# Kernel optimization log

Hardware: AMD Instinct MI355X
Metric: run time of the kernel (lower is better)

Reference implementation:

```python
import jax, jax.numpy as jnp
import numpy as np

P = 128; D = 128; A = 128
NS = D * A            # sinogram nodes
NP = P * P            # pixel nodes
N = NS + NP           # total graph nodes
EPS = 1e-5
_PNAMES = ["af_w1","af_b1","af_p1","af_bn_g","af_bn_b","af_w2","af_b2","af_p2","af_w3","af_b3","af_p3","af_w4","af_b4","af_p4","af_w5","af_b5","af_p5","gcn_w","gcn_b","sr_w1","sr_b1","sr_p1","sr_w2","sr_b2","sr_p2","sr_w3","sr_b3","sr_p3"]


def _conv(x, w, b, pad):
    y = jax.lax.conv_general_dilated(x, w, (1, 1), [(pad, pad), (pad, pad)],
                                     dimension_numbers=("NCHW", "OIHW", "NCHW"))
    return y + b[None, :, None, None]


def _prelu(x, a):
    return jnp.where(x >= 0, x, a * x)


def _bn(x, g, b):
    # BatchNorm2d in training mode: biased batch stats over (N,H,W)
    m = x.mean(axis=(0, 2, 3), keepdims=True)
    v = x.var(axis=(0, 2, 3), keepdims=True)
    return (x - m) * jax.lax.rsqrt(v + EPS) * g[None, :, None, None] + b[None, :, None, None]


def _forward(sino, edge_index, edge_weight, p):
    # AndrewCNN sinogram filter: 1 -> 64 -> 64 -> 64 -> 64 -> 8, 7x7 convs
    h = _prelu(_conv(sino, p["af_w1"], p["af_b1"], 3), p["af_p1"])
    h = _bn(h, p["af_bn_g"], p["af_bn_b"])
    h = _prelu(_conv(h, p["af_w2"], p["af_b2"], 3), p["af_p2"])
    h = _prelu(_conv(h, p["af_w3"], p["af_b3"], 3), p["af_p3"])
    h = _prelu(_conv(h, p["af_w4"], p["af_b4"], 3), p["af_p4"])
    h = _prelu(_conv(h, p["af_w5"], p["af_b5"], 3), p["af_p5"])   # [B,8,D,A]
    B, F = h.shape[0], h.shape[1]
    # build_nodes_features (source_to_target): sino nodes first, zero pixel nodes
    flat_sino = h.transpose(0, 2, 3, 1).reshape(B, NS, F)
    x = jnp.concatenate([flat_sino, jnp.zeros((B, NP, F), h.dtype)], axis=1)  # [B,N,8]
    # GCNConv(8,10): lin -> gcn_norm with self loops -> scatter-add at targets -> +bias
    xl = x @ p["gcn_w"]                                            # [B,N,10]
    row, col = edge_index[0], edge_index[1]
    loop = jnp.arange(N)
    row2 = jnp.concatenate([row, loop])
    col2 = jnp.concatenate([col, loop])
    w2 = jnp.concatenate([edge_weight, jnp.ones((N,), edge_weight.dtype)])
    deg = jnp.zeros((N,), xl.dtype).at[col2].add(w2)
    dis = jnp.where(deg > 0, jax.lax.rsqrt(jnp.maximum(deg, EPS * 0 + 1e-30)), 0.0)
    norm = dis[row2] * w2 * dis[col2]                              # [E+N]
    msgs = xl[:, row2, :] * norm[None, :, None]                    # [B,E+N,10]
    agg = jnp.zeros_like(xl).at[:, col2, :].add(msgs) + p["gcn_b"]
    # keep pixel nodes, reshape to image grid
    img = agg[:, NS:, :].transpose(0, 2, 1).reshape(B, -1, P, P)   # [B,10,P,P]
    # SRNET: 10 -> 64 (9x9) -> 32 (1x1) -> 1 (5x5)
    o = _prelu(_conv(img, p["sr_w1"], p["sr_b1"], 4), p["sr_p1"])
    o = _prelu(_conv(o,   p["sr_w2"], p["sr_b2"], 0), p["sr_p2"])
    o = _prelu(_conv(o,   p["sr_w3"], p["sr_b3"], 2), p["sr_p3"])
    return o


def setup_inputs() -> dict:
    f = jnp.float32
    ks = jax.random.split(jax.random.key(0), 16)
    B, E = 4, 2097152
    def rn(k, shape, s):
        return jax.random.normal(k, shape, f) * s
    inp = {
        "sino": jax.random.normal(ks[0], (B, 1, D, A), f),
        "edge_index": jax.random.randint(ks[1], (2, E), 0, N),
        "edge_weight": jax.random.uniform(ks[2], (E,), f),
    }
    kw = jax.random.split(ks[3], 9)
    inp["af_w1"] = rn(kw[0], (64, 1, 7, 7), 0.2)
    inp["af_w2"] = rn(kw[1], (64, 64, 7, 7), 0.03)
    inp["af_w3"] = rn(kw[2], (64, 64, 7, 7), 0.03)
    inp["af_w4"] = rn(kw[3], (64, 64, 7, 7), 0.03)
    inp["af_w5"] = rn(kw[4], (8, 64, 7, 7), 0.03)
    inp["gcn_w"] = rn(kw[5], (8, 10), 0.3)
    inp["sr_w1"] = rn(kw[6], (64, 10, 9, 9), 0.05)
    inp["sr_w2"] = rn(kw[7], (32, 64, 1, 1), 0.18)
    inp["sr_w3"] = rn(kw[8], (1, 32, 5, 5), 0.05)
    for nm, c in [("af_b1", 64), ("af_b2", 64), ("af_b3", 64), ("af_b4", 64), ("af_b5", 8), ("sr_b1", 64), ("sr_b2", 32), ("sr_b3", 1)]:
        inp[nm] = jnp.zeros((c,), f)
    inp["gcn_b"] = jnp.zeros((10,), f)
    inp["af_bn_g"] = jnp.ones((64,), f)
    inp["af_bn_b"] = jnp.zeros((64,), f)
    for nm in ["af_p1", "af_p2", "af_p3", "af_p4", "af_p5", "sr_p1", "sr_p2", "sr_p3"]:
        inp[nm] = jnp.array(0.25, f)
    return inp


def reference(sino, edge_index, edge_weight, af_w1, af_b1, af_p1, af_bn_g, af_bn_b, af_w2, af_b2, af_p2, af_w3, af_b3, af_p3, af_w4, af_b4, af_p4, af_w5, af_b5, af_p5, gcn_w, gcn_b, sr_w1, sr_b1, sr_p1, sr_w2, sr_b2, sr_p2, sr_w3, sr_b3, sr_p3):
    p = dict(zip(_PNAMES, (af_w1, af_b1, af_p1, af_bn_g, af_bn_b, af_w2, af_b2, af_p2, af_w3, af_b3, af_p3, af_w4, af_b4, af_p4, af_w5, af_b5, af_p5, gcn_w, gcn_b, sr_w1, sr_b1, sr_p1, sr_w2, sr_b2, sr_p2, sr_w3, sr_b3, sr_p3)))
    return _forward(sino, edge_index, edge_weight, p)
```

## Files before the change

### kernel.cpp

```cpp
#include <hip/hip_runtime.h>

static constexpr int NS = 16384;

typedef __attribute__((ext_vector_type(8))) short bf16x8;
typedef __attribute__((ext_vector_type(4))) float f32x4;

__device__ inline unsigned short bf16_rne(float x) {
  unsigned u = __float_as_uint(x);
  unsigned r = u + 0x7FFF + ((u >> 16) & 1);
  return (unsigned short)(r >> 16);
}

__global__ void k_wtrans(const float* __restrict__ w, float* __restrict__ wT,
                         int CO, int CI_IN, int CI_OUT, int KS) {
  int i = blockIdx.x * 256 + threadIdx.x;
  int tot = KS * KS * CI_OUT * CO;
  if (i >= tot) return;
  int co = i % CO;
  int r = i / CO;
  int ci = r % CI_OUT;
  int t = r / CI_OUT;
  int ky = t / KS, kx = t % KS;
  float v = 0.f;
  if (ci < CI_IN) v = w[((co * CI_IN + ci) * KS + ky) * KS + kx];
  wT[i] = v;
}

__global__ void k_wpack(const float* __restrict__ w, unsigned short* __restrict__ wpk) {
  int i = blockIdx.x * 256 + threadIdx.x;
  if (i >= 49 * 64 * 64) return;
  int co = i & 63, r = i >> 6;
  int ci = r & 63, tap = r >> 6;
  float v = w[(co * 64 + ci) * 49 + tap];
  unsigned short hi = bf16_rne(v);
  float hif = __uint_as_float((unsigned)hi << 16);
  unsigned short lo = bf16_rne(v - hif);
  int ks = ci >> 5, k32 = ci & 31;
  int lane = ((k32 >> 3) << 4) | (co & 15);
  int j = ci & 7, nt = co >> 4;
  size_t base = ((size_t)(((tap * 2 + ks) * 4 + nt) * 2) * 64 + lane) * 8 + j;
  wpk[base] = hi;
  wpk[base + 512] = lo;
}

__global__ void k_wpacks(const float* __restrict__ sw1,
                         unsigned short* __restrict__ wpk) {
  int i = blockIdx.x * 256 + threadIdx.x;
  if (i >= 360 * 512) return;
  int j = i & 7, l = (i >> 3) & 63, f = i >> 9;
  int sp = f & 1, nt = (f >> 1) & 3;
  int r3 = f >> 3, p = r3 % 5, ky = r3 / 5;
  int co = nt * 16 + (l & 15);
  int k = ((l >> 4) << 3) + j;
  int kx = 2 * p + (k >> 4);
  int ci = k & 15;
  float v = (ci < 10 && kx < 9) ? sw1[((co * 10 + ci) * 9 + ky) * 9 + kx] : 0.f;
  unsigned short hi = bf16_rne(v);
  unsigned short outv;
  if (sp == 0) {
    outv = hi;
  } else {
    float hif = __uint_as_float((unsigned)hi << 16);
    outv = bf16_rne(v - hif);
  }
  wpk[i] = outv;
}

__global__ __launch_bounds__(128) void k_conv1(
    const float* __restrict__ sino, const float* __restrict__ wT1,
    const float* __restrict__ b1, const float* __restrict__ p1,
    float* __restrict__ out) {
  int b = blockIdx.x >> 7, y = blockIdx.x & 127, x = threadIdx.x;
  float acc[64];
#pragma unroll
  for (int i = 0; i < 64; ++i) acc[i] = 0.f;
#pragma unroll
  for (int ky = 0; ky < 7; ++ky) {
    int yy = y + ky - 3;
#pragma unroll
    for (int kx = 0; kx < 7; ++kx) {
      int xx = x + kx - 3;
      float v = (yy >= 0 && yy < 128 && xx >= 0 && xx < 128)
                    ? sino[(b * 128 + yy) * 128 + xx]
                    : 0.f;
      const float* wr = wT1 + (ky * 7 + kx) * 64;
#pragma unroll
      for (int co = 0; co < 64; ++co) acc[co] += v * wr[co];
    }
  }
  float a = p1[0];
  float* op = out + ((size_t)(b * 134 + y + 3) * 134 + x + 3) * 64;
#pragma unroll
  for (int co = 0; co < 64; ++co) {
    float v = acc[co] + b1[co];
    op[co] = v >= 0.f ? v : a * v;
  }
}

__global__ __launch_bounds__(256) void k_bnstats(const float* __restrict__ x1p,
                                                 double* __restrict__ bnsum) {
  int c = threadIdx.x & 63, sl = threadIdx.x >> 6;
  double s = 0.0, q = 0.0;
  int base = blockIdx.x * 512 + sl * 128;
  for (int i = 0; i < 128; ++i) {
    int p = base + i;
    int b = p >> 14, y = (p >> 7) & 127, x = p & 127;
    double v = (double)x1p[((size_t)(b * 134 + y + 3) * 134 + x + 3) * 64 + c];
    s += v;
    q += v * v;
  }
  __shared__ double red[2][4][64];
  red[0][sl][c] = s;
  red[1][sl][c] = q;
  __syncthreads();
  if (sl == 0) {
    s = red[0][0][c] + red[0][1][c] + red[0][2][c] + red[0][3][c];
    q = red[1][0][c] + red[1][1][c] + red[1][2][c] + red[1][3][c];
    atomicAdd(&bnsum[c], s);
    atomicAdd(&bnsum[64 + c], q);
  }
}

__global__ void k_bnfinal(const double* __restrict__ bnsum, float* __restrict__ bnsc,
                          const float* __restrict__ g, const float* __restrict__ bb) {
  int c = threadIdx.x;
  if (c >= 64) return;
  double m = bnsum[c] * (1.0 / 65536.0);
  double v = bnsum[64 + c] * (1.0 / 65536.0) - m * m;
  double sc = (double)g[c] * rsqrt(v + 1e-5);
  bnsc[c] = (float)sc;
  bnsc[64 + c] = (float)((double)bb[c] - m * sc);
}

__global__ __launch_bounds__(256) void k_bnapply(float* __restrict__ x1p,
                                                 const float* __restrict__ bnsc) {
  int i = blockIdx.x * 256 + threadIdx.x;
  if (i >= 4 * 128 * 128 * 16) return;
  int g = i & 15, p = i >> 4;
  int b = p >> 14, y = (p >> 7) & 127, x = p & 127;
  float* ptr = x1p + ((size_t)(b * 134 + y + 3) * 134 + x + 3) * 64 + g * 4;
  float4 v = *(float4*)ptr;
  int c = g * 4;
  v.x = v.x * bnsc[c + 0] + bnsc[64 + c + 0];
  v.y = v.y * bnsc[c + 1] + bnsc[64 + c + 1];
  v.z = v.z * bnsc[c + 2] + bnsc[64 + c + 2];
  v.w = v.w * bnsc[c + 3] + bnsc[64 + c + 3];
  *(float4*)ptr = v;
}

__global__ __launch_bounds__(256) void k_convm(
    const float* __restrict__ in, const unsigned short* __restrict__ wpk,
    const float* __restrict__ bias, const float* __restrict__ alpha,
    float* __restrict__ out) {
  int b = blockIdx.x >> 7, y = blockIdx.x & 127;
  int tid = threadIdx.x, l = tid & 63;
  int wv = tid >> 6;
  int pxb = (wv & 1) * 64;
  int coh = wv >> 1;
  int lg = l >> 4, lm = l & 15;

  __shared__ unsigned short hbuf[2][134 * 40];
  __shared__ unsigned short lbuf[2][134 * 40];

  f32x4 acc[4][2];
#pragma unroll
  for (int mt = 0; mt < 4; ++mt)
#pragma unroll
    for (int ntl = 0; ntl < 2; ++ntl) acc[mt][ntl] = (f32x4){0.f, 0.f, 0.f, 0.f};

  for (int ch = 0; ch < 64; ch += 32) {
    auto stage = [&](int ky, int s) {
      const float* gin = in + ((size_t)(b * 134 + y + ky) * 134) * 64 + ch;
      for (int i = tid; i < 134 * 8; i += 256) {
        int px = i >> 3, q = i & 7;
        float4 v = *(const float4*)(gin + px * 64 + q * 4);
        unsigned short h0 = bf16_rne(v.x), h1 = bf16_rne(v.y);
        unsigned short h2 = bf16_rne(v.z), h3 = bf16_rne(v.w);
        unsigned short l0 = bf16_rne(v.x - __uint_as_float((unsigned)h0 << 16));
        unsigned short l1 = bf16_rne(v.y - __uint_as_float((unsigned)h1 << 16));
        unsigned short l2 = bf16_rne(v.z - __uint_as_float((unsigned)h2 << 16));
        unsigned short l3 = bf16_rne(v.w - __uint_as_float((unsigned)h3 << 16));
        *(ushort4*)&hbuf[s][px * 40 + q * 4] = make_ushort4(h0, h1, h2, h3);
        *(ushort4*)&lbuf[s][px * 40 + q * 4] = make_ushort4(l0, l1, l2, l3);
      }
    };
    stage(0, 0);
    __syncthreads();
    for (int ky = 0; ky < 7; ++ky) {
      if (ky < 6) stage(ky + 1, (ky + 1) & 1);
      int s = ky & 1;
#pragma unroll
      for (int kx = 0; kx < 7; ++kx) {
        int tap = ky * 7 + kx;
        const unsigned short* wt =
            wpk + (size_t)(tap * 2 + (ch >> 5)) * 8 * 512 + (size_t)l * 8;
        bf16x8 Bh[2], Bl[2];
#pragma unroll
        for (int ntl = 0; ntl < 2; ++ntl) {
          int nt = coh * 2 + ntl;
          Bh[ntl] = *(const bf16x8*)(wt + (nt * 2 + 0) * 512);
          Bl[ntl] = *(const bf16x8*)(wt + (nt * 2 + 1) * 512);
        }
#pragma unroll
        for (int mt = 0; mt < 4; ++mt) {
          int px = pxb + mt * 16 + lm + kx;
          bf16x8 Ah = *(const bf16x8*)&hbuf[s][px * 40 + lg * 8];
          bf16x8 Al = *(const bf16x8*)&lbuf[s][px * 40 + lg * 8];
#pragma unroll
          for (int ntl = 0; ntl < 2; ++ntl) {
            acc[mt][ntl] = __builtin_amdgcn_mfma_f32_16x16x32_bf16(Ah, Bh[ntl],
                                                                   acc[mt][ntl], 0, 0, 0);
            acc[mt][ntl] = __builtin_amdgcn_mfma_f32_16x16x32_bf16(Ah, Bl[ntl],
                                                                   acc[mt][ntl], 0, 0, 0);
            acc[mt][ntl] = __builtin_amdgcn_mfma_f32_16x16x32_bf16(Al, Bh[ntl],
                                                                   acc[mt][ntl], 0, 0, 0);
          }
        }
      }
      __syncthreads();
    }
  }
  float a = alpha[0];
#pragma unroll
  for (int mt = 0; mt < 4; ++mt)
#pragma unroll
    for (int ntl = 0; ntl < 2; ++ntl)
#pragma unroll
      for (int r = 0; r < 4; ++r) {
        int px = pxb + mt * 16 + lg * 4 + r;
        int co = coh * 32 + ntl * 16 + lm;
        float v = acc[mt][ntl][r] + bias[co];
        out[((size_t)(b * 134 + y + 3) * 134 + px + 3) * 64 + co] =
            v >= 0.f ? v : a * v;
      }
}

__global__ __launch_bounds__(256) void k_convs(
    const float* __restrict__ imgp, const unsigned short* __restrict__ wpk,
    const float* __restrict__ bias, const float* __restrict__ alpha,
    float* __restrict__ out) {
  int b = blockIdx.x >> 7, y = blockIdx.x & 127;
  int tid = threadIdx.x, l = tid & 63;
  int wv = tid >> 6, wbase = wv * 32;
  int lg = l >> 4, lm = l & 15;

  __shared__ unsigned short hbuf[2][137 * 20];
  __shared__ unsigned short lbuf[2][137 * 20];

  f32x4 acc[2][4];
#pragma unroll
  for (int mt = 0; mt < 2; ++mt)
#pragma unroll
    for (int nt = 0; nt < 4; ++nt) acc[mt][nt] = (f32x4){0.f, 0.f, 0.f, 0.f};

  auto stage = [&](int ky, int s) {
    const float* gin = imgp + ((size_t)(b * 136 + y + ky) * 136) * 16;
    for (int i = tid; i < 137 * 4; i += 256) {
      int px = i >> 2, q = i & 3;
      float4 v = (px < 136) ? *(const float4*)(gin + px * 16 + q * 4)
                            : make_float4(0.f, 0.f, 0.f, 0.f);
      unsigned short h0 = bf16_rne(v.x), h1 = bf16_rne(v.y);
      unsigned short h2 = bf16_rne(v.z), h3 = bf16_rne(v.w);
      unsigned short l0 = bf16_rne(v.x - __uint_as_float((unsigned)h0 << 16));
      unsigned short l1 = bf16_rne(v.y - __uint_as_float((unsigned)h1 << 16));
      unsigned short l2 = bf16_rne(v.z - __uint_as_float((unsigned)h2 << 16));
      unsigned short l3 = bf16_rne(v.w - __uint_as_float((unsigned)h3 << 16));
      *(ushort4*)&hbuf[s][px * 20 + q * 4] = make_ushort4(h0, h1, h2, h3);
      *(ushort4*)&lbuf[s][px * 20 + q * 4] = make_ushort4(l0, l1, l2, l3);
    }
  };
  stage(0, 0);
  __syncthreads();
  for (int ky = 0; ky < 9; ++ky) {
    if (ky < 8) stage(ky + 1, (ky + 1) & 1);
    int s = ky & 1;
#pragma unroll
    for (int p = 0; p < 5; ++p) {
      const unsigned short* wt =
          wpk + ((size_t)(ky * 5 + p) * 8) * 512 + (size_t)l * 8;
      bf16x8 Bh[4], Bl[4];
#pragma unroll
      for (int nt = 0; nt < 4; ++nt) {
        Bh[nt] = *(const bf16x8*)(wt + (nt * 2 + 0) * 512);
        Bl[nt] = *(const bf16x8*)(wt + (nt * 2 + 1) * 512);
      }
#pragma unroll
      for (int mt = 0; mt < 2; ++mt) {
        int px = wbase + mt * 16 + lm + 2 * p + (lg >> 1);
        bf16x8 Ah = *(const bf16x8*)&hbuf[s][px * 20 + (lg & 1) * 8];
        bf16x8 Al = *(const bf16x8*)&lbuf[s][px * 20 + (lg & 1) * 8];
#pragma unroll
        for (int nt = 0; nt < 4; ++nt) {
          acc[mt][nt] =
              __builtin_amdgcn_mfma_f32_16x16x32_bf16(Ah, Bh[nt], acc[mt][nt], 0, 0, 0);
          acc[mt][nt] =
              __builtin_amdgcn_mfma_f32_16x16x32_bf16(Ah, Bl[nt], acc[mt][nt], 0, 0, 0);
          acc[mt][nt] =
              __builtin_amdgcn_mfma_f32_16x16x32_bf16(Al, Bh[nt], acc[mt][nt], 0, 0, 0);
        }
      }
    }
    __syncthreads();
  }
  float a = alpha[0];
#pragma unroll
  for (int mt = 0; mt < 2; ++mt)
#pragma unroll
    for (int nt = 0; nt < 4; ++nt)
#pragma unroll
      for (int r = 0; r < 4; ++r) {
        int px = wbase + mt * 16 + lg * 4 + r;
        int co = nt * 16 + lm;
        float v = acc[mt][nt][r] + bias[co];
        out[((size_t)(b * 128 + y) * 128 + px) * 64 + co] = v >= 0.f ? v : a * v;
      }
}

template <int CIN, int COUT, int KS, int IN_H, int IN_W, int OUT_H, int OUT_W,
          int OUT_OFF, int STR, int CH, int NSPLIT>
__global__ __launch_bounds__(64 * NSPLIT) void k_conv3(
    const float* __restrict__ in, const float* __restrict__ wT,
    const float* __restrict__ bias, const float* __restrict__ alpha,
    float* __restrict__ out) {
  constexpr int C = COUT / NSPLIT;
  int b = blockIdx.x >> 6, y0 = (blockIdx.x & 63) * 2;
  int l = threadIdx.x & 63;
  int cob = __builtin_amdgcn_readfirstlane((int)(threadIdx.x >> 6) * C);
  __shared__ float sbuf[2][IN_W * STR];
  float acc[4][C];
#pragma unroll
  for (int r = 0; r < 4; ++r)
#pragma unroll
    for (int i = 0; i < C; ++i) acc[r][i] = 0.f;

  for (int ch = 0; ch < CIN; ch += CH) {
    auto stage = [&](int k) {
      const float* gin = in + ((size_t)(b * IN_H + y0 + k) * IN_W) * CIN + ch;
      float* dst = sbuf[k & 1];
      constexpr int N4 = IN_W * CH / 4;
      for (int i = threadIdx.x; i < N4; i += 64 * NSPLIT) {
        int xx = i / (CH / 4), c4 = (i - xx * (CH / 4)) * 4;
        float4 v = *(const float4*)(gin + (size_t)xx * CIN + c4);
        *(float4*)(dst + xx * STR + c4) = v;
      }
    };
    stage(0);
    stage(1);
    __syncthreads();
    for (int ky = 0; ky < KS; ++ky) {
      const float* sA = sbuf[ky & 1];
      const float* sB = sbuf[(ky + 1) & 1];
      for (int kx = 0; kx < KS; ++kx) {
        const float* wt = wT + ((size_t)(ky * KS + kx) * CIN + ch) * COUT + cob;
        const float* a0p = sA + (l + kx) * STR;
        const float* a1p = sA + (l + 64 + kx) * STR;
        const float* b0p = sB + (l + kx) * STR;
        const float* b1p = sB + (l + 64 + kx) * STR;
#pragma unroll
        for (int ci = 0; ci < CH; ci += 4) {
          float4 a0 = *(const float4*)(a0p + ci);
          float4 a1 = *(const float4*)(a1p + ci);
          float4 b0 = *(const float4*)(b0p + ci);
          float4 b1 = *(const float4*)(b1p + ci);
#pragma unroll
          for (int c = 0; c < 4; ++c) {
            const float* wr = wt + (size_t)(ci + c) * COUT;
            float va0 = ((const float*)&a0)[c], va1 = ((const float*)&a1)[c];
            float vb0 = ((const float*)&b0)[c], vb1 = ((const float*)&b1)[c];
#pragma unroll
            for (int co = 0; co < C; ++co) {
              float w = wr[co];
              acc[0][co] += va0 * w;
              acc[1][co] += va1 * w;
              acc[2][co] += vb0 * w;
              acc[3][co] += vb1 * w;
            }
          }
        }
      }
      __syncthreads();
      if (ky < KS - 1) {
        stage(ky + 2);
        __syncthreads();
      }
    }
  }
  float a = alpha[0];
#pragma unroll
  for (int r = 0; r < 2; ++r) {
    float* rowp =
        out + (((size_t)(b * OUT_H + y0 + r + OUT_OFF)) * OUT_W + OUT_OFF) * COUT + cob;
#pragma unroll
    for (int p = 0; p < 2; ++p) {
      float* op = rowp + (size_t)(l + p * 64) * COUT;
#pragma unroll
      for (int co = 0; co < C; ++co) {
        float v = acc[r * 2 + p][co] + bias[cob + co];
        op[co] = v >= 0.f ? v : a * v;
      }
    }
  }
}

template <int CIN, int COUT, int KS, int IN_H, int IN_W, int OUT_H, int OUT_W,
          int OUT_OFF, int STR, int NSPLIT>
__global__ __launch_bounds__(64 * NSPLIT) void k_conv2(
    const float* __restrict__ in, const float* __restrict__ wT,
    const float* __restrict__ bias, const float* __restrict__ alpha,
    float* __restrict__ out) {
  constexpr int C = COUT / NSPLIT;
  int b = blockIdx.x >> 7, y = blockIdx.x & 127;
  int l = threadIdx.x & 63;
  int cob = __builtin_amdgcn_readfirstlane((int)(threadIdx.x >> 6) * C);
  __shared__ float srow[IN_W * STR];
  float acc0[C], acc1[C];
#pragma unroll
  for (int i = 0; i < C; ++i) acc0[i] = acc1[i] = 0.f;

  for (int ky = 0; ky < KS; ++ky) {
    __syncthreads();
    const float* gin = in + (size_t)(b * IN_H + y + ky) * IN_W * CIN;
    constexpr int N4 = IN_W * CIN / 4;
    for (int i = threadIdx.x; i < N4; i += 64 * NSPLIT) {
      float4 v = *(const float4*)(gin + (size_t)i * 4);
      int xx = (i * 4) / CIN, cc = (i * 4) % CIN;
      *(float4*)(srow + xx * STR + cc) = v;
    }
    __syncthreads();
    for (int kx = 0; kx < KS; ++kx) {
      const float* wt = wT + ((size_t)(ky * KS + kx) * CIN) * COUT + cob;
      const float* s0 = srow + (l + kx) * STR;
      const float* s1 = srow + (l + 64 + kx) * STR;
      for (int ci = 0; ci < CIN; ci += 4) {
        float4 a0 = *(const float4*)(s0 + ci);
        float4 a1 = *(const float4*)(s1 + ci);
#pragma unroll
        for (int c = 0; c < 4; ++c) {
          float v0 = ((const float*)&a0)[c];
          float v1 = ((const float*)&a1)[c];
          const float* wr = wt + (size_t)(ci + c) * COUT;
#pragma unroll
          for (int co = 0; co < C; ++co) {
            float w = wr[co];
            acc0[co] += v0 * w;
            acc1[co] += v1 * w;
          }
        }
      }
    }
  }
  float a = alpha[0];
  float* rowp = out + ((size_t)(b * OUT_H + y + OUT_OFF) * OUT_W + OUT_OFF) * COUT + cob;
  float* op0 = rowp + (size_t)l * COUT;
  float* op1 = rowp + (size_t)(l + 64) * COUT;
#pragma unroll
  for (int co = 0; co < C; ++co) {
    float bi = bias[cob + co];
    float v0 = acc0[co] + bi;
    float v1 = acc1[co] + bi;
    op0[co] = v0 >= 0.f ? v0 : a * v0;
    op1[co] = v1 >= 0.f ? v1 : a * v1;
  }
}

__global__ __launch_bounds__(512, 4) void k_conv5gcn(
    const float* __restrict__ in, const float* __restrict__ wT5,
    const float* __restrict__ b5, const float* __restrict__ p5,
    const float* __restrict__ gw, float* __restrict__ xl) {
  int b = blockIdx.x >> 7, y = blockIdx.x & 127;
  int x = threadIdx.x & 127;
  int cig = __builtin_amdgcn_readfirstlane((int)(threadIdx.x >> 7));
  __shared__ float srow[134 * 68];
  __shared__ float red[4][128][8];
  float acc[8];
#pragma unroll
  for (int i = 0; i < 8; ++i) acc[i] = 0.f;

  for (int ky = 0; ky < 7; ++ky) {
    __syncthreads();
    const float* gin = in + (size_t)(b * 134 + y + ky) * 134 * 64;
    for (int i = threadIdx.x; i < 134 * 64; i += 512) {
      int xx = i >> 6, cc = i & 63;
      srow[xx * 68 + cc] = gin[i];
    }
    __syncthreads();
    for (int kx = 0; kx < 7; ++kx) {
      const float* wt = wT5 + (size_t)(ky * 7 + kx) * 64 * 8 + cig * 16 * 8;
      const float* sr = srow + (x + kx) * 68 + cig * 16;
#pragma unroll
      for (int ci = 0; ci < 16; ci += 4) {
        float4 iv = *(const float4*)(sr + ci);
#pragma unroll
        for (int c = 0; c < 4; ++c) {
          float vv = ((const float*)&iv)[c];
          const float* wr = wt + (ci + c) * 8;
#pragma unroll
          for (int co = 0; co < 8; ++co) acc[co] += vv * wr[co];
        }
      }
    }
  }
#pragma unroll
  for (int co = 0; co < 8; ++co) red[cig][x][co] = acc[co];
  __syncthreads();
  if (cig == 0) {
    float a = p5[0];
    float feat[8];
#pragma unroll
    for (int co = 0; co < 8; ++co) {
      float v = red[0][x][co] + red[1][x][co] + red[2][x][co] + red[3][x][co] + b5[co];
      feat[co] = v >= 0.f ? v : a * v;
    }
    float o[10];
#pragma unroll
    for (int f = 0; f < 10; ++f) o[f] = 0.f;
#pragma unroll
    for (int c = 0; c < 8; ++c) {
#pragma unroll
      for (int f = 0; f < 10; ++f) o[f] += feat[c] * gw[c * 10 + f];
    }
    float* op = xl + ((size_t)b * 16384 + y * 128 + x) * 10;
#pragma unroll
    for (int f = 0; f < 10; ++f) op[f] = o[f];
  }
}

template <int HALF>
__global__ __launch_bounds__(1024) void k_degp(
    const int* __restrict__ ei, const float* __restrict__ ew,
    float* __restrict__ pdeg, int* __restrict__ cnt, int* __restrict__ rank, int E) {
  __shared__ float degl[16384];
  for (int i = threadIdx.x; i < 16384; i += 1024) degl[i] = 0.f;
  __syncthreads();
  int chunk = (E + gridDim.x - 1) / gridDim.x;
  int base = blockIdx.x * chunk;
  int end = min(E, base + chunk);
  for (int e = base + (int)threadIdx.x; e < end; e += 1024) {
    int col = ei[E + e];
    float w = ew[e];
    if ((col >> 14) == HALF) atomicAdd(&degl[col & 16383], w);
    if (HALF == 1) {
      int row = ei[e];
      if (row < NS && col >= NS) rank[e] = atomicAdd(&cnt[col - NS], 1);
    }
  }
  __syncthreads();
  float* pd = pdeg + (size_t)blockIdx.x * 16384;
  for (int i = threadIdx.x; i < 16384; i += 1024) pd[i] = degl[i];
}

__global__ void k_dis2(const float* __restrict__ pdegA, const float* __restrict__ pdegB,
                       float* __restrict__ dis, int nb) {
  int n = blockIdx.x * 256 + threadIdx.x;
  if (n >= 2 * NS) return;
  const float* p = (n < NS ? pdegA : pdegB) + (n & 16383);
  float s = 1.0f;
  for (int b = 0; b < nb; ++b) s += p[(size_t)b * 16384];
  dis[n] = rsqrtf(s);
}

__global__ __launch_bounds__(1024) void k_scan(const int* __restrict__ cnt,
                                               int* __restrict__ ptr) {
  __shared__ int ps[1024];
  int tid = threadIdx.x;
  int base = tid * 16;
  int v[16];
  int s = 0;
#pragma unroll
  for (int k = 0; k < 16; ++k) {
    v[k] = s;
    s += cnt[base + k];
  }
  ps[tid] = s;
  __syncthreads();
  for (int off = 1; off < 1024; off <<= 1) {
    int t = (tid >= off) ? ps[tid - off] : 0;
    __syncthreads();
    ps[tid] += t;
    __syncthreads();
  }
  int chunkoff = (tid == 0) ? 0 : ps[tid - 1];
#pragma unroll
  for (int k = 0; k < 16; ++k) ptr[base + k] = chunkoff + v[k];
  if (tid == 1023) ptr[16384] = ps[1023];
}

__global__ void k_bucket2(const int* __restrict__ ei, const float* __restrict__ ew,
                          const float* __restrict__ dis, const int* __restrict__ ptr,
                          const int* __restrict__ rank, int* __restrict__ erow,
                          float* __restrict__ enrm, int E) {
  int e = blockIdx.x * 256 + threadIdx.x;
  if (e >= E) return;
  int row = ei[e], col = ei[E + e];
  if (row >= NS || col < NS) return;
  int cp = col - NS;
  int pos = ptr[cp] + rank[e];
  erow[pos] = row;
  enrm[pos] = dis[row] * ew[e] * dis[col];
}

__global__ __launch_bounds__(256) void k_gather(
    const int* __restrict__ ptr, const int* __restrict__ erow,
    const float* __restrict__ enrm, const float* __restrict__ xl,
    const float* __restrict__ gb, float* __restrict__ imgp) {
  int cp = blockIdx.x * 4 + (threadIdx.x >> 6);
  int l = threadIdx.x & 63;
  int b = l >> 4, f = l & 15;
  bool act = f < 10;
  float acc = 0.f;
  int s = ptr[cp], e1 = ptr[cp + 1];
  for (int e = s; e < e1; ++e) {
    int row = erow[e];
    float nrm = enrm[e];
    if (act) acc += xl[((size_t)b * 16384 + row) * 10 + f] * nrm;
  }
  if (act) {
    int y = cp >> 7, x = cp & 127;
    imgp[((size_t)(b * 136 + y + 4) * 136 + x + 4) * 16 + f] = acc + gb[f];
  }
}

extern "C" void kernel_launch(void* const* d_in, const int* in_sizes, int n_in,
                              void* d_out, int out_size, void* d_ws, size_t ws_size,
                              hipStream_t stream) {
  const float* sino = (const float*)d_in[0];
  const int* ei = (const int*)d_in[1];
  const float* ew = (const float*)d_in[2];
  const float* w1 = (const float*)d_in[3];
  const float* w2 = (const float*)d_in[4];
  const float* w3 = (const float*)d_in[5];
  const float* w4 = (const float*)d_in[6];
  const float* w5 = (const float*)d_in[7];
  const float* gw = (const float*)d_in[8];
  const float* sw1 = (const float*)d_in[9];
  const float* sw2 = (const float*)d_in[10];
  const float* sw3 = (const float*)d_in[11];
  const float* b1 = (const float*)d_in[12];
  const float* b2 = (const float*)d_in[13];
  const float* b3 = (const float*)d_in[14];
  const float* b4 = (const float*)d_in[15];
  const float* b5 = (const float*)d_in[16];
  const float* sb1 = (const float*)d_in[17];
  const float* sb2 = (const float*)d_in[18];
  const float* sb3 = (const float*)d_in[19];
  const float* gb = (const float*)d_in[20];
  const float* bng = (const float*)d_in[21];
  const float* bnb = (const float*)d_in[22];
  const float* p1 = (const float*)d_in[23];
  const float* p2 = (const float*)d_in[24];
  const float* p3 = (const float*)d_in[25];
  const float* p4 = (const float*)d_in[26];
  const float* p5 = (const float*)d_in[27];
  const float* sp1 = (const float*)d_in[28];
  const float* sp2 = (const float*)d_in[29];
  const float* sp3 = (const float*)d_in[30];
  const int E = in_sizes[2];

  char* ws = (char*)d_ws;
  size_t off = 0;
  auto alloc = [&](size_t bytes) {
    char* p = ws + off;
    off += (bytes + 255) & ~(size_t)255;
    return p;
  };
  float* x1p = (float*)alloc((size_t)4 * 134 * 134 * 64 * 4);
  float* x2p = (float*)alloc((size_t)4 * 134 * 134 * 64 * 4);
  unsigned short* wpk2 = (unsigned short*)alloc(401408 * 2);
  unsigned short* wpk3 = (unsigned short*)alloc(401408 * 2);
  unsigned short* wpk4 = (unsigned short*)alloc(401408 * 2);
  unsigned short* wpks1 = (unsigned short*)alloc(184320 * 2);
  float* wt1 = (float*)alloc(3136 * 4);
  float* wt5 = (float*)alloc(25088 * 4);
  float* wts2 = (float*)alloc(2048 * 4);
  float* wts3 = (float*)alloc(800 * 4);
  double* bnsum = (double*)alloc(128 * 8);
  float* bnsc = (float*)alloc(128 * 4);
  float* xl = (float*)alloc((size_t)4 * 16384 * 10 * 4);
  float* pdegA = (float*)alloc((size_t)128 * 16384 * 4);
  float* pdegB = (float*)alloc((size_t)128 * 16384 * 4);
  float* dis = (float*)alloc(32768 * 4);
  int* cnt = (int*)alloc(16384 * 4);
  int* ptr = (int*)alloc(16385 * 4);
  int* rank = (int*)alloc((size_t)E * 4);
  int* erow = (int*)alloc((size_t)E * 4);
  float* enrm = (float*)alloc((size_t)E * 4);
  float* imgp = (float*)alloc((size_t)4 * 136 * 136 * 16 * 4);
  float* s1 = (float*)alloc((size_t)4 * 128 * 128 * 64 * 4);
  float* s2p = (float*)alloc((size_t)4 * 132 * 132 * 32 * 4);

  hipMemsetAsync(x1p, 0, (size_t)4 * 134 * 134 * 64 * 4, stream);
  hipMemsetAsync(x2p, 0, (size_t)4 * 134 * 134 * 64 * 4, stream);
  hipMemsetAsync(bnsum, 0, 128 * 8, stream);
  hipMemsetAsync(cnt, 0, 16384 * 4, stream);
  hipMemsetAsync(imgp, 0, (size_t)4 * 136 * 136 * 16 * 4, stream);
  hipMemsetAsync(s2p, 0, (size_t)4 * 132 * 132 * 32 * 4, stream);

  k_wpack<<<784, 256, 0, stream>>>(w2, wpk2);
  k_wpack<<<784, 256, 0, stream>>>(w3, wpk3);
  k_wpack<<<784, 256, 0, stream>>>(w4, wpk4);
  k_wpacks<<<720, 256, 0, stream>>>(sw1, wpks1);
  k_wtrans<<<13, 256, 0, stream>>>(w1, wt1, 64, 1, 1, 7);
  k_wtrans<<<98, 256, 0, stream>>>(w5, wt5, 8, 64, 64, 7);
  k_wtrans<<<8, 256, 0, stream>>>(sw2, wts2, 32, 64, 64, 1);
  k_wtrans<<<4, 256, 0, stream>>>(sw3, wts3, 1, 32, 32, 5);

  k_conv1<<<512, 128, 0, stream>>>(sino, wt1, b1, p1, x1p);
  k_bnstats<<<128, 256, 0, stream>>>(x1p, bnsum);
  k_bnfinal<<<1, 64, 0, stream>>>(bnsum, bnsc, bng, bnb);
  k_bnapply<<<4096, 256, 0, stream>>>(x1p, bnsc);

  k_convm<<<512, 256, 0, stream>>>(x1p, wpk2, b2, p2, x2p);
  k_convm<<<512, 256, 0, stream>>>(x2p, wpk3, b3, p3, x1p);
  k_convm<<<512, 256, 0, stream>>>(x1p, wpk4, b4, p4, x2p);
  k_conv5gcn<<<512, 512, 0, stream>>>(x2p, wt5, b5, p5, gw, xl);

  k_degp<0><<<128, 1024, 0, stream>>>(ei, ew, pdegA, cnt, rank, E);
  k_degp<1><<<128, 1024, 0, stream>>>(ei, ew, pdegB, cnt, rank, E);
  k_dis2<<<128, 256, 0, stream>>>(pdegA, pdegB, dis, 128);
  k_scan<<<1, 1024, 0, stream>>>(cnt, ptr);
  k_bucket2<<<(E + 255) / 256, 256, 0, stream>>>(ei, ew, dis, ptr, rank, erow, enrm, E);
  k_gather<<<4096, 256, 0, stream>>>(ptr, erow, enrm, xl, gb, imgp);

  k_convs<<<512, 256, 0, stream>>>(imgp, wpks1, sb1, sp1, s1);
  k_conv3<64, 32, 1, 128, 128, 132, 132, 2, 36, 32, 8>
      <<<256, 512, 0, stream>>>(s1, wts2, sb2, sp2, s2p);
  k_conv2<32, 1, 5, 132, 132, 128, 128, 0, 36, 1>
      <<<512, 64, 0, stream>>>(s2p, wts3, sb3, sp3, (float*)d_out);
}
```

Measured before the change: 670.1 us.

## Move conv5 (64->8, 7x7) onto bf16x3 MFMA with split-precision weight packing

Replaces the scalar FP32 conv5+GCN-linear kernel with an MFMA kernel. Inputs are split into bf16 hi/lo parts in double-buffered shared memory, and three 16x16x32 bf16 MFMAs per tap emulate fp32 accuracy. Output channels are padded from 8 to 16, so half of the MFMA columns are wasted. Adds a new weight-packing kernel, and the per-row staging conversion adds ALU work.

```diff
diff --git a/kernel.cpp b/kernel.cpp
--- a/kernel.cpp
+++ b/kernel.cpp
@@ -41,6 +41,28 @@
   size_t base = ((size_t)(((tap * 2 + ks) * 4 + nt) * 2) * 64 + lane) * 8 + j;
   wpk[base] = hi;
   wpk[base + 512] = lo;
+}
+
+__global__ void k_wpack5(const float* __restrict__ w5,
+                         unsigned short* __restrict__ wpk) {
+  int i = blockIdx.x * 256 + threadIdx.x;
+  if (i >= 196 * 512) return;
+  int j = i & 7, l = (i >> 3) & 63, f = i >> 9;
+  int sp = f & 1, r = f >> 1;
+  int ks = r & 1, tap = r >> 1;
+  int co = l & 15;
+  int k32 = ((l >> 4) << 3) + j;
+  int ci = ks * 32 + k32;
+  float v = (co < 8) ? w5[(co * 64 + ci) * 49 + tap] : 0.f;
+  unsigned short hi = bf16_rne(v);
+  unsigned short outv;
+  if (sp == 0) {
+    outv = hi;
+  } else {
+    float hif = __uint_as_float((unsigned)hi << 16);
+    outv = bf16_rne(v - hif);
+  }
+  wpk[i] = outv;
 }
 
 __global__ void k_wpacks(const float* __restrict__ sw1,
@@ -235,6 +257,94 @@
       }
 }
 
+__global__ __launch_bounds__(256) void k_convm5(
+    const float* __restrict__ in, const unsigned short* __restrict__ wpk,
+    const float* __restrict__ b5, const float* __restrict__ p5,
+    const float* __restrict__ gw, float* __restrict__ xl) {
+  int b = blockIdx.x >> 7, y = blockIdx.x & 127;
+  int tid = threadIdx.x, l = tid & 63;
+  int wv = tid >> 6;
+  int pxb = wv * 32;
+  int lg = l >> 4, lm = l & 15;
+
+  __shared__ unsigned short hbuf[2][134 * 40];
+  __shared__ unsigned short lbuf[2][134 * 40];
+  __shared__ float feat[128][9];
+
+  f32x4 acc[2];
+  acc[0] = (f32x4){0.f, 0.f, 0.f, 0.f};
+  acc[1] = (f32x4){0.f, 0.f, 0.f, 0.f};
+
+  for (int ch = 0; ch < 64; ch += 32) {
+    auto stage = [&](int ky, int s) {
+      const float* gin = in + ((size_t)(b * 134 + y + ky) * 134) * 64 + ch;
+      for (int i = tid; i < 134 * 8; i += 256) {
+        int px = i >> 3, q = i & 7;
+        float4 v = *(const float4*)(gin + px * 64 + q * 4);
+        unsigned short h0 = bf16_rne(v.x), h1 = bf16_rne(v.y);
+        unsigned short h2 = bf16_rne(v.z), h3 = bf16_rne(v.w);
+        unsigned short l0 = bf16_rne(v.x - __uint_as_float((unsigned)h0 << 16));
+        unsigned short l1 = bf16_rne(v.y - __uint_as_float((unsigned)h1 << 16));
+        unsigned short l2 = bf16_rne(v.z - __uint_as_float((unsigned)h2 << 16));
+        unsigned short l3 = bf16_rne(v.w - __uint_as_float((unsigned)h3 << 16));
+        *(ushort4*)&hbuf[s][px * 40 + q * 4] = make_ushort4(h0, h1, h2, h3);
+        *(ushort4*)&lbuf[s][px * 40 + q * 4] = make_ushort4(l0, l1, l2, l3);
+      }
+    };
+    stage(0, 0);
+    __syncthreads();
+    for (int ky = 0; ky < 7; ++ky) {
+      if (ky < 6) stage(ky + 1, (ky + 1) & 1);
+      int s = ky & 1;
+#pragma unroll
+      for (int kx = 0; kx < 7; ++kx) {
+        int tap = ky * 7 + kx;
+        const unsigned short* wt =
+            wpk + (size_t)((tap * 2 + (ch >> 5)) * 2) * 512 + (size_t)l * 8;
+        bf16x8 Bh = *(const bf16x8*)(wt);
+        bf16x8 Bl = *(const bf16x8*)(wt + 512);
+#pragma unroll
+        for (int mt = 0; mt < 2; ++mt) {
+          int px = pxb + mt * 16 + lm + kx;
+          bf16x8 Ah = *(const bf16x8*)&hbuf[s][px * 40 + lg * 8];
+          bf16x8 Al = *(const bf16x8*)&lbuf[s][px * 40 + lg * 8];
+          acc[mt] = __builtin_amdgcn_mfma_f32_16x16x32_bf16(Ah, Bh, acc[mt], 0, 0, 0);
+          acc[mt] = __builtin_amdgcn_mfma_f32_16x16x32_bf16(Ah, Bl, acc[mt], 0, 0, 0);
+          acc[mt] = __builtin_amdgcn_mfma_f32_16x16x32_bf16(Al, Bh, acc[mt], 0, 0, 0);
+        }
+      }
+      __syncthreads();
+    }
+  }
+  float a = p5[0];
+  if (lm < 8) {
+#pragma unroll
+    for (int mt = 0; mt < 2; ++mt)
+#pragma unroll
+      for (int r = 0; r < 4; ++r) {
+        int px = pxb + mt * 16 + lg * 4 + r;
+        float v = acc[mt][r] + b5[lm];
+        feat[px][lm] = v >= 0.f ? v : a * v;
+      }
+  }
+  __syncthreads();
+  if (tid < 128) {
+    int px = tid;
+    float o[10];
+#pragma unroll
+    for (int f = 0; f < 10; ++f) o[f] = 0.f;
+#pragma unroll
+    for (int c = 0; c < 8; ++c) {
+      float fv = feat[px][c];
+#pragma unroll
+      for (int f = 0; f < 10; ++f) o[f] += fv * gw[c * 10 + f];
+    }
+    float* op = xl + ((size_t)b * 16384 + y * 128 + px) * 10;
+#pragma unroll
+    for (int f = 0; f < 10; ++f) op[f] = o[f];
+  }
+}
+
 __global__ __launch_bounds__(256) void k_convs(
     const float* __restrict__ imgp, const unsigned short* __restrict__ wpk,
     const float* __restrict__ bias, const float* __restrict__ alpha,
@@ -460,68 +570,6 @@
     float v1 = acc1[co] + bi;
     op0[co] = v0 >= 0.f ? v0 : a * v0;
     op1[co] = v1 >= 0.f ? v1 : a * v1;
-  }
-}
-
-__global__ __launch_bounds__(512, 4) void k_conv5gcn(
-    const float* __restrict__ in, const float* __restrict__ wT5,
-    const float* __restrict__ b5, const float* __restrict__ p5,
-    const float* __restrict__ gw, float* __restrict__ xl) {
-  int b = blockIdx.x >> 7, y = blockIdx.x & 127;
-  int x = threadIdx.x & 127;
-  int cig = __builtin_amdgcn_readfirstlane((int)(threadIdx.x >> 7));
-  __shared__ float srow[134 * 68];
-  __shared__ float red[4][128][8];
-  float acc[8];
-#pragma unroll
-  for (int i = 0; i < 8; ++i) acc[i] = 0.f;
-
-  for (int ky = 0; ky < 7; ++ky) {
-    __syncthreads();
-    const float* gin = in + (size_t)(b * 134 + y + ky) * 134 * 64;
-    for (int i = threadIdx.x; i < 134 * 64; i += 512) {
-      int xx = i >> 6, cc = i & 63;
-      srow[xx * 68 + cc] = gin[i];
-    }
-    __syncthreads();
-    for (int kx = 0; kx < 7; ++kx) {
-      const float* wt = wT5 + (size_t)(ky * 7 + kx) * 64 * 8 + cig * 16 * 8;
-      const float* sr = srow + (x + kx) * 68 + cig * 16;
-#pragma unroll
-      for (int ci = 0; ci < 16; ci += 4) {
-        float4 iv = *(const float4*)(sr + ci);
-#pragma unroll
-        for (int c = 0; c < 4; ++c) {
-          float vv = ((const float*)&iv)[c];
-          const float* wr = wt + (ci + c) * 8;
-#pragma unroll
-          for (int co = 0; co < 8; ++co) acc[co] += vv * wr[co];
-        }
-      }
-    }
-  }
-#pragma unroll
-  for (int co = 0; co < 8; ++co) red[cig][x][co] = acc[co];
-  __syncthreads();
-  if (cig == 0) {
-    float a = p5[0];
-    float feat[8];
-#pragma unroll
-    for (int co = 0; co < 8; ++co) {
-      float v = red[0][x][co] + red[1][x][co] + red[2][x][co] + red[3][x][co] + b5[co];
-      feat[co] = v >= 0.f ? v : a * v;
-    }
-    float o[10];
-#pragma unroll
-    for (int f = 0; f < 10; ++f) o[f] = 0.f;
-#pragma unroll
-    for (int c = 0; c < 8; ++c) {
-#pragma unroll
-      for (int f = 0; f < 10; ++f) o[f] += feat[c] * gw[c * 10 + f];
-    }
-    float* op = xl + ((size_t)b * 16384 + y * 128 + x) * 10;
-#pragma unroll
-    for (int f = 0; f < 10; ++f) op[f] = o[f];
   }
 }
 
@@ -668,9 +716,9 @@
   unsigned short* wpk2 = (unsigned short*)alloc(401408 * 2);
   unsigned short* wpk3 = (unsigned short*)alloc(401408 * 2);
   unsigned short* wpk4 = (unsigned short*)alloc(401408 * 2);
+  unsigned short* wpk5 = (unsigned short*)alloc(100352 * 2);
   unsigned short* wpks1 = (unsigned short*)alloc(184320 * 2);
   float* wt1 = (float*)alloc(3136 * 4);
-  float* wt5 = (float*)alloc(25088 * 4);
   float* wts2 = (float*)alloc(2048 * 4);
   float* wts3 = (float*)alloc(800 * 4);
   double* bnsum = (double*)alloc(128 * 8);
@@ -698,9 +746,9 @@
   k_wpack<<<784, 256, 0, stream>>>(w2, wpk2);
   k_wpack<<<784, 256, 0, stream>>>(w3, wpk3);
   k_wpack<<<784, 256, 0, stream>>>(w4, wpk4);
+  k_wpack5<<<392, 256, 0, stream>>>(w5, wpk5);
   k_wpacks<<<720, 256, 0, stream>>>(sw1, wpks1);
   k_wtrans<<<13, 256, 0, stream>>>(w1, wt1, 64, 1, 1, 7);
-  k_wtrans<<<98, 256, 0, stream>>>(w5, wt5, 8, 64, 64, 7);
   k_wtrans<<<8, 256, 0, stream>>>(sw2, wts2, 32, 64, 64, 1);
   k_wtrans<<<4, 256, 0, stream>>>(sw3, wts3, 1, 32, 32, 5);
 
@@ -712,7 +760,7 @@
   k_convm<<<512, 256, 0, stream>>>(x1p, wpk2, b2, p2, x2p);
   k_convm<<<512, 256, 0, stream>>>(x2p, wpk3, b3, p3, x1p);
   k_convm<<<512, 256, 0, stream>>>(x1p, wpk4, b4, p4, x2p);
-  k_conv5gcn<<<512, 512, 0, stream>>>(x2p, wt5, b5, p5, gw, xl);
+  k_convm5<<<512, 256, 0, stream>>>(x2p, wpk5, b5, p5, gw, xl);
 
   k_degp<0><<<128, 1024, 0, stream>>>(ei, ew, pdegA, cnt, rank, E);
   k_degp<1><<<128, 1024, 0, stream>>>(ei, ew, pdegB, cnt, rank, E);
```

New measurement: 661.4 us. Within noise of the previous version (-1.3%).
